# Performance work log

Hardware: AMD Instinct MI355X
Metric: run time of the kernel (lower is better)

Reference implementation:

```python
import jax, jax.numpy as jnp
import numpy as np

A, K, CIN, H, W = 8, 50, 64, 100, 352
C1, C2, C3, COUT = 128, 128, 256, 256


def setup_inputs() -> dict:
    key = jax.random.key(0)
    ks = jax.random.split(key, 16)

    def mkw(k, o, i, kh, kw):
        k1, k2 = jax.random.split(k)
        scale = (2.0 / (i * kh * kw)) ** 0.5 * 0.5  # damped He init to keep 8-layer relu stack stable
        return (jax.random.normal(k1, (o, i, kh, kw), jnp.float32) * scale,
                jax.random.normal(k2, (o,), jnp.float32) * 0.01)

    w1a, b1a = mkw(ks[0], C1, CIN, 3, 3)
    w1b, b1b = mkw(ks[1], C1, C1, 3, 3)
    w2a, b2a = mkw(ks[2], C2, C1, 3, 3)
    w2b, b2b = mkw(ks[3], C2, C2, 3, 3)
    w3a, b3a = mkw(ks[4], C3, C2, 3, 3)
    w3b, b3b = mkw(ks[5], C3, C3, 3, 3)
    wDa, bDa = mkw(ks[6], C3, C3, 3, 3)
    wDb, bDb = mkw(ks[7], COUT, C3, 1, 1)
    wF, bF = mkw(ks[8], COUT, COUT, 1, 1)

    feature = jax.random.normal(ks[9], (A, CIN, H, W), jnp.float32)

    # integer BEV boxes (left, right, up, down), right>left, down>up, vehicle-scale extents
    l = jax.random.randint(ks[10], (A, K), 0, W - 17)
    bw = jax.random.randint(ks[11], (A, K), 4, 17)
    u = jax.random.randint(ks[12], (A, K), 0, H - 17)
    bh = jax.random.randint(ks[13], (A, K), 4, 17)
    boxes = jnp.stack([l, l + bw, u, u + bh], axis=-1).astype(jnp.int32)  # [A,K,4]

    return dict(feature=feature, boxes=boxes,
                w1a=w1a, b1a=b1a, w1b=w1b, b1b=b1b,
                w2a=w2a, b2a=b2a, w2b=w2b, b2b=b2b,
                w3a=w3a, b3a=b3a, w3b=w3b, b3b=b3b,
                wDa=wDa, bDa=bDa, wDb=wDb, bDb=bDb,
                wF=wF, bF=bF)


def _conv(x, w, b, pad):
    y = jax.lax.conv_general_dilated(x, w, (1, 1), [(pad, pad), (pad, pad)],
                                     dimension_numbers=('NCHW', 'OIHW', 'NCHW'))
    return y + b[None, :, None, None]


def _superbox(feature, boxes, w1a, b1a, w1b, b1b, w2a, b2a, w2b, b2b,
              w3a, b3a, w3b, b3b, wDa, bDa, wDb, bDb, wF, bF):
    x = feature
    for (wi, bi) in ((w1a, b1a), (w1b, b1b), (w2a, b2a), (w2b, b2b),
                     (w3a, b3a), (w3b, b3b), (wDa, bDa)):
        x = jax.nn.relu(_conv(x, wi, bi, 1))
    x = jax.nn.relu(_conv(x, wDb, bDb, 0))        # [A,256,H,W] features_matching

    # get_box_feature: pool(relu(finalconv(crop))). finalconv is 1x1 (pointwise),
    # so this equals the box-mean of relu(finalconv(full map)) -> integral image.
    y = jax.nn.relu(_conv(x, wF, bF, 0))          # [A,256,H,W]
    S = jnp.pad(jnp.cumsum(jnp.cumsum(y, axis=2), axis=3),
                ((0, 0), (0, 0), (1, 0), (1, 0)))  # [A,256,H+1,W+1] integral image

    l, r, u, d = boxes[..., 0], boxes[..., 1], boxes[..., 2], boxes[..., 3]  # each [A,K]

    def agent_pool(Sa, la, ra, ua, da):
        # Sa: [C,H+1,W+1]; adjacent advanced indices -> [C,K]
        tot = Sa[:, da, ra] - Sa[:, ua, ra] - Sa[:, da, la] + Sa[:, ua, la]
        area = ((da - ua) * (ra - la)).astype(Sa.dtype)
        return (tot / area).T                     # [K,C]

    desc = jax.vmap(agent_pool)(S, l, r, u, d)    # [A,K,256]
    return desc


def reference(feature, boxes, w1a, b1a, w1b, b1b, w2a, b2a, w2b, b2b,
              w3a, b3a, w3b, b3b, wDa, bDa, wDb, bDb, wF, bF):
    return _superbox(feature, boxes, w1a, b1a, w1b, b1b, w2a, b2a, w2b, b2b,
                     w3a, b3a, w3b, b3b, wDa, bDa, wDb, bDb, wF, bF)
```

## Files before the change

kernel.cpp:

```cpp
#include <hip/hip_runtime.h>
#include <hip/hip_bf16.h>

typedef unsigned int u32;
typedef unsigned short u16;
typedef __attribute__((ext_vector_type(8))) short bf16x8;
typedef __attribute__((ext_vector_type(4))) float f32x4;

#define DEVI __device__ __forceinline__

constexpr int AG = 8, H = 100, W = 352, HP = 102, WP = 354;
constexpr int HWp = H * W;
constexpr int NB = 2 * WP + 2 * H;

DEVI u16 f2bf(float f) {
  __hip_bfloat16 h = __float2bfloat16(f);
  return *reinterpret_cast<u16*>(&h);
}
DEVI float bf2f(u16 v) { return __uint_as_float(((u32)v) << 16); }

DEVI int chperm(int j) { int v = j >> 3, r = j & 7; return (r < 4) ? 4 * v + r : 16 + 4 * v + (r - 4); }
DEVI int chlog(int c) { return (c & ~31) + chperm(c & 31); }

DEVI int xcd_lin(int orig, int nwg) {
  int q = nwg >> 3, r8 = nwg & 7;
  int xcd = orig & 7, pos = orig >> 3;
  return (xcd < r8 ? xcd * (q + 1) : r8 * (q + 1) + (xcd - r8) * q) + pos;
}

typedef __attribute__((address_space(1))) const u32 as1c_u32;
typedef __attribute__((address_space(3))) u32 as3_u32;
DEVI void gload16(const u16* g, u16* l) {
  __builtin_amdgcn_global_load_lds((as1c_u32*)(const void*)g, (as3_u32*)(void*)l, 16, 0, 0);
}

template <int N> DEVI void waitcnt_vm() {
  if constexpr (N == 0) asm volatile("s_waitcnt vmcnt(0)" ::: "memory");
  else if constexpr (N == 3) asm volatile("s_waitcnt vmcnt(3)" ::: "memory");
  else if constexpr (N == 4) asm volatile("s_waitcnt vmcnt(4)" ::: "memory");
  else asm volatile("s_waitcnt vmcnt(0)" ::: "memory");
}

__global__ void convert_feat(const float* __restrict__ f, u16* __restrict__ dst) {
  __shared__ float t32[64][33];
  int blk = blockIdx.x;
  int wseg = blk % 11;
  int rest = blk / 11;
  int h = rest % H;
  int a = rest / H;
  int t = threadIdx.x;
  int wbase = wseg * 32;
  {
    int w = t & 31;
    int c0 = (t >> 5) * 8;
#pragma unroll
    for (int i = 0; i < 8; ++i) {
      int lc = c0 + i;
      t32[lc][w] = f[((size_t)(a * 64 + lc) * H + h) * W + wbase + w];
    }
  }
  __syncthreads();
  int p = t >> 3;
  int cs = (t & 7) * 8;
  u16 tmp[8];
#pragma unroll
  for (int j = 0; j < 8; ++j) {
    int c = cs + j;
    int lc = (c & 32) + chperm(c & 31);
    tmp[j] = f2bf(t32[lc][p]);
  }
  size_t ob = ((size_t)(a * HP + h + 1) * WP + (wbase + p + 1)) * 64 + cs;
  *reinterpret_cast<uint4*>(dst + ob) = *reinterpret_cast<uint4*>(tmp);
}

template <int C>
__global__ void zero_border(u16* __restrict__ buf, int nA) {
  constexpr int CH = C / 8;
  int idx = blockIdx.x * 256 + threadIdx.x;
  int pix = idx / CH;
  int cc = (idx - pix * CH) * 8;
  if (pix >= nA * NB) return;
  int a = pix / NB;
  int b = pix - a * NB;
  int h, w;
  if (b < WP) { h = 0; w = b; }
  else if (b < 2 * WP) { h = HP - 1; w = b - WP; }
  else {
    int bb = b - 2 * WP;
    int bb2 = (bb < H) ? bb : bb - H;
    h = 1 + bb2;
    w = (bb < H) ? 0 : (WP - 1);
  }
  size_t off = ((size_t)(a * HP + h) * WP + w) * C + cc;
  *reinterpret_cast<uint4*>(buf + off) = make_uint4(0u, 0u, 0u, 0u);
}

__global__ void repack_w(const float* __restrict__ w, u16* __restrict__ rp,
                         int O, int I, int taps) {
  int idx = blockIdx.x * 256 + threadIdx.x;
  int total = O * I * taps;
  if (idx >= total) return;
  int jj = idx & 7;
  int u = (idx >> 3) & 7;
  int r = (idx >> 6) % O;
  int s = idx / (O * 64);
  int KB = I >> 6;
  int kb = s % KB;
  int t = s / KB;
  int lu = u ^ (r & 7);
  int g = lu & 3, j32 = lu >> 2;
  int cp = (jj < 4) ? 4 * g + jj : 16 + 4 * g + (jj - 4);
  int i = kb * 64 + j32 * 32 + cp;
  int o = (r & ~31) + chperm(r & 31);
  rp[idx] = f2bf(w[((size_t)o * I + i) * taps + t]);
}

__global__ void repack_plain(const float* __restrict__ w, u16* __restrict__ rp) {
  int idx = blockIdx.x * 256 + threadIdx.x;
  int jj = idx & 7;
  int g = (idx >> 3) & 3;
  int r = (idx >> 5) & 255;
  int kb = idx >> 13;
  int cp = (jj < 4) ? 4 * g + jj : 16 + 4 * g + (jj - 4);
  int i = kb * 32 + cp;
  int o = chlog(r);
  rp[idx] = f2bf(w[(size_t)o * 256 + i]);
}

template <int CIN, int COUT, int MAXCH, int HALO>
__global__ __launch_bounds__(256, 2) void conv_boxk(
    const u16* __restrict__ in, const u16* __restrict__ wrp,
    const float* __restrict__ bias, u16* __restrict__ out,
    const int* __restrict__ boxes) {
  constexpr int BM = 128, BN = 128, BK = 64, TAPS = 9;
  constexpr int KB = CIN / BK;
  constexpr int KS = TAPS * KB;
  constexpr int NT = 256;
  constexpr int NC = COUT / BN;
  constexpr int ACH = 4, AH = 2, BH = 2, HALF = 4;
  constexpr int ASZ = BM * BK;
  constexpr int BSZ = BN * BK;
  __shared__ u16 smem[2 * (ASZ + BSZ)];

  const int blk = xcd_lin(blockIdx.x, gridDim.x);
  const int cb = blk % NC;
  const int t1 = blk / NC;
  const int c0 = t1 % MAXCH;
  const int box = t1 / MAXCH;
  const int* bx = boxes + box * 4;
  const int a = box / 50;
  const int cl = max(bx[0] - HALO, 0);
  const int cr = min(bx[1] + HALO, W);
  const int r0 = max(bx[2] - HALO, 0);
  const int r1 = min(bx[3] + HALO, H);
  const int bw = cr - cl;
  const int npx = bw * (r1 - r0);
  if (c0 * 128 >= npx) return;

  const int tid = threadIdx.x;
  const int lane = tid & 63;
  const int wid = tid >> 6;
  const int wr = wid >> 1;
  const int wc = wid & 1;

  int aoff[ACH];
#pragma unroll
  for (int i = 0; i < ACH; ++i) {
    int c = tid + i * NT;
    int p = c >> 3, u = c & 7;
    int lu = u ^ (p & 7);
    int idx = c0 * 128 + p;
    if (idx >= npx) idx = npx - 1;
    int ph = r0 + idx / bw;
    int pw = cl + idx % bw;
    aoff[i] = ((a * HP + ph + 1) * WP + (pw + 1)) * CIN + lu * 8;
  }

  f32x4 acc[4][4];
#pragma unroll
  for (int m = 0; m < 4; ++m)
#pragma unroll
    for (int n = 0; n < 4; ++n) acc[m][n] = f32x4{0.f, 0.f, 0.f, 0.f};

  const int g = lane >> 4;
  const int arow = lane & 15;
  const int fk = arow & 7;

  auto stage = [&](int s, int h) {
    int par = s & 1;
    u16* Ad = smem + par * ASZ;
    u16* Bd = smem + 2 * ASZ + par * BSZ;
    int t = s / KB;
    int kb = s - t * KB;
    int doff = kb * BK + ((t / 3 - 1) * WP + (t % 3 - 1)) * CIN;
    const u16* wtile = wrp + (size_t)s * (COUT * BK) + cb * BSZ;
#pragma unroll
    for (int i = h * AH; i < h * AH + AH; ++i)
      gload16(in + aoff[i] + doff, Ad + (tid + i * NT) * 8);
#pragma unroll
    for (int i = h * BH; i < h * BH + BH; ++i)
      gload16(wtile + (tid + i * NT) * 8, Bd + (tid + i * NT) * 8);
  };

  stage(0, 0);
  stage(0, 1);

  for (int s = 0; s < KS; ++s) {
    int par = s & 1;
    const u16* Ab = smem + par * ASZ;
    const u16* Bb = smem + 2 * ASZ + par * BSZ;
    if (s + 1 < KS) {
      stage(s + 1, 0);
      waitcnt_vm<HALF>();
    } else {
      waitcnt_vm<0>();
    }
    __builtin_amdgcn_s_barrier();

#pragma unroll
    for (int j = 0; j < 2; ++j) {
      bf16x8 af[4], bfr[4];
#pragma unroll
      for (int m = 0; m < 4; ++m)
        af[m] = *reinterpret_cast<const bf16x8*>(
            Ab + (wr * 64 + m * 16 + arow) * 64 + (((j * 4 + g) ^ fk) << 3));
#pragma unroll
      for (int n = 0; n < 4; ++n)
        bfr[n] = *reinterpret_cast<const bf16x8*>(
            Bb + (wc * 64 + n * 16 + arow) * 64 + (((j * 4 + g) ^ fk) << 3));
      __builtin_amdgcn_s_setprio(1);
#pragma unroll
      for (int m = 0; m < 4; ++m)
#pragma unroll
        for (int n = 0; n < 4; ++n)
          acc[m][n] = __builtin_amdgcn_mfma_f32_16x16x32_bf16(af[m], bfr[n], acc[m][n], 0, 0, 0);
      __builtin_amdgcn_s_setprio(0);
      if (j == 0 && s + 1 < KS) stage(s + 1, 1);
    }
    __builtin_amdgcn_s_barrier();
  }

  __syncthreads();
  float bs[4];
#pragma unroll
  for (int n = 0; n < 4; ++n) bs[n] = bias[chlog(cb * BN + wc * 64 + n * 16 + arow)];
  u16* et = smem + wid * 2048;
#pragma unroll
  for (int pp = 0; pp < 2; ++pp) {
    if (pp) __syncthreads();
#pragma unroll
    for (int mm = 0; mm < 2; ++mm) {
      int m = pp * 2 + mm;
#pragma unroll
      for (int rg = 0; rg < 4; ++rg) {
        int row = mm * 16 + g * 4 + rg;
#pragma unroll
        for (int n = 0; n < 4; ++n) {
          int col = (n * 16 + arow) ^ (g << 4);
          et[row * 64 + col] = f2bf(fmaxf(acc[m][n][rg] + bs[n], 0.f));
        }
      }
    }
    __syncthreads();
#pragma unroll
    for (int jj = 0; jj < 4; ++jj) {
      int p = jj * 8 + (lane >> 3);
      int un = lane & 7;
      int su = un ^ (((p >> 2) & 3) << 1);
      uint4 qv = *reinterpret_cast<const uint4*>(et + p * 64 + su * 8);
      int idx = c0 * 128 + wr * 64 + pp * 32 + p;
      if (idx >= npx) idx = npx - 1;
      int ph = r0 + idx / bw;
      int pw = cl + idx % bw;
      size_t ob = ((size_t)(a * HP + ph + 1) * WP + (pw + 1)) * COUT +
                  cb * BN + wc * 64 + un * 8;
      *reinterpret_cast<uint4*>(out + ob) = qv;
    }
  }
}

template <int CIN, int EOUT, int MAXCH, int MODE>
__global__ __launch_bounds__(256, 2) void conv_tl(
    const u16* __restrict__ in, const u16* __restrict__ wrp,
    const float* __restrict__ bias, u16* __restrict__ out,
    const int* __restrict__ boxes) {
  constexpr int BM = 128, BN = 128, BK = 64, TAPS = 9;
  constexpr int KB = CIN / BK;
  constexpr int KS = TAPS * KB;
  constexpr int NT = 256;
  constexpr int NC = 2;
  constexpr int COUT = 256;
  constexpr int ACH = 4, AH = 2, BH = 2, HALF = 4;
  constexpr int ASZ = BM * BK;
  constexpr int BSZ = BN * BK;
  constexpr int TSLOT = (MODE == 0) ? 400 : (MODE == 1) ? 324 : 256;
  constexpr int TIN_SLOT = (MODE == 1) ? 400 : (MODE == 2) ? 324 : 0;
  __shared__ u16 smem[2 * (ASZ + BSZ)];

  const int blk = xcd_lin(blockIdx.x, gridDim.x);
  const int cb = blk % NC;
  const int t1 = blk / NC;
  const int c0 = t1 % MAXCH;
  const int box = t1 / MAXCH;
  const int* bx = boxes + box * 4;
  const int a = box / 50;
  const int bw = bx[1] - bx[0], bh = bx[3] - bx[2];
  const int bwO = bw + 2 * EOUT, bhO = bh + 2 * EOUT;
  const int NPX = bwO * bhO;
  if (c0 * 128 >= NPX) return;
  const int org_r = bx[2] - EOUT, org_c = bx[0] - EOUT;
  const int bwIn = bw + 2 * (EOUT + 1);

  const int tid = threadIdx.x;
  const int lane = tid & 63;
  const int wid = tid >> 6;
  const int wr = wid >> 1;
  const int wc = wid & 1;

  const u16* src = (MODE == 0) ? in : in + (size_t)box * TIN_SLOT * CIN;

  int aoff[ACH];
#pragma unroll
  for (int i = 0; i < ACH; ++i) {
    int c = tid + i * NT;
    int p = c >> 3, u = c & 7;
    int lu = u ^ (p & 7);
    int idx = c0 * 128 + p;
    if (idx >= NPX) idx = NPX - 1;
    int r = idx / bwO, cc = idx - r * bwO;
    if (MODE == 0) {
      int mr = org_r + r, mc = org_c + cc;
      mr = min(max(mr, 0), H - 1);
      mc = min(max(mc, 0), W - 1);
      aoff[i] = ((a * HP + mr + 1) * WP + (mc + 1)) * CIN + lu * 8;
    } else {
      aoff[i] = ((r + 1) * bwIn + (cc + 1)) * CIN + lu * 8;
    }
  }

  f32x4 acc[4][4];
#pragma unroll
  for (int m = 0; m < 4; ++m)
#pragma unroll
    for (int n = 0; n < 4; ++n) acc[m][n] = f32x4{0.f, 0.f, 0.f, 0.f};

  const int g = lane >> 4;
  const int arow = lane & 15;
  const int fk = arow & 7;
  const int stride = (MODE == 0) ? WP : bwIn;

  auto stage = [&](int s, int h) {
    int par = s & 1;
    u16* Ad = smem + par * ASZ;
    u16* Bd = smem + 2 * ASZ + par * BSZ;
    int t = s / KB;
    int kb = s - t * KB;
    int doff = kb * BK + ((t / 3 - 1) * stride + (t % 3 - 1)) * CIN;
    const u16* wtile = wrp + (size_t)s * (COUT * BK) + cb * BSZ;
#pragma unroll
    for (int i = h * AH; i < h * AH + AH; ++i)
      gload16(src + aoff[i] + doff, Ad + (tid + i * NT) * 8);
#pragma unroll
    for (int i = h * BH; i < h * BH + BH; ++i)
      gload16(wtile + (tid + i * NT) * 8, Bd + (tid + i * NT) * 8);
  };

  stage(0, 0);
  stage(0, 1);

  for (int s = 0; s < KS; ++s) {
    int par = s & 1;
    const u16* Ab = smem + par * ASZ;
    const u16* Bb = smem + 2 * ASZ + par * BSZ;
    if (s + 1 < KS) {
      stage(s + 1, 0);
      waitcnt_vm<HALF>();
    } else {
      waitcnt_vm<0>();
    }
    __builtin_amdgcn_s_barrier();

#pragma unroll
    for (int j = 0; j < 2; ++j) {
      bf16x8 af[4], bfr[4];
#pragma unroll
      for (int m = 0; m < 4; ++m)
        af[m] = *reinterpret_cast<const bf16x8*>(
            Ab + (wr * 64 + m * 16 + arow) * 64 + (((j * 4 + g) ^ fk) << 3));
#pragma unroll
      for (int n = 0; n < 4; ++n)
        bfr[n] = *reinterpret_cast<const bf16x8*>(
            Bb + (wc * 64 + n * 16 + arow) * 64 + (((j * 4 + g) ^ fk) << 3));
      __builtin_amdgcn_s_setprio(1);
#pragma unroll
      for (int m = 0; m < 4; ++m)
#pragma unroll
        for (int n = 0; n < 4; ++n)
          acc[m][n] = __builtin_amdgcn_mfma_f32_16x16x32_bf16(af[m], bfr[n], acc[m][n], 0, 0, 0);
      __builtin_amdgcn_s_setprio(0);
      if (j == 0 && s + 1 < KS) stage(s + 1, 1);
    }
    __builtin_amdgcn_s_barrier();
  }

  __syncthreads();
  float bs[4];
#pragma unroll
  for (int n = 0; n < 4; ++n) bs[n] = bias[chlog(cb * BN + wc * 64 + n * 16 + arow)];
  u16* et = smem + wid * 2048;
#pragma unroll
  for (int pp = 0; pp < 2; ++pp) {
    if (pp) __syncthreads();
#pragma unroll
    for (int mm = 0; mm < 2; ++mm) {
      int m = pp * 2 + mm;
#pragma unroll
      for (int rg = 0; rg < 4; ++rg) {
        int row = mm * 16 + g * 4 + rg;
#pragma unroll
        for (int n = 0; n < 4; ++n) {
          int col = (n * 16 + arow) ^ (g << 4);
          et[row * 64 + col] = f2bf(fmaxf(acc[m][n][rg] + bs[n], 0.f));
        }
      }
    }
    __syncthreads();
#pragma unroll
    for (int jj = 0; jj < 4; ++jj) {
      int p = jj * 8 + (lane >> 3);
      int un = lane & 7;
      int su = un ^ (((p >> 2) & 3) << 1);
      uint4 qv = *reinterpret_cast<const uint4*>(et + p * 64 + su * 8);
      int idx = c0 * 128 + wr * 64 + pp * 32 + p;
      if (idx >= NPX) idx = NPX - 1;
      if (MODE != 2) {
        int r2 = idx / bwO, c2 = idx - (idx / bwO) * bwO;
        int mr = org_r + r2, mc = org_c + c2;
        if (mr < 0 || mr >= H || mc < 0 || mc >= W)
          qv = make_uint4(0u, 0u, 0u, 0u);
      }
      size_t ob = ((size_t)box * TSLOT + idx) * COUT + cb * BN + wc * 64 + un * 8;
      *reinterpret_cast<uint4*>(out + ob) = qv;
    }
  }
}

__global__ __launch_bounds__(256) void fuse_box(
    const u16* __restrict__ x, const u16* __restrict__ wDbp,
    const float* __restrict__ bDb, const u16* __restrict__ wFp,
    const float* __restrict__ bF, const int* __restrict__ boxes,
    float* __restrict__ desc) {
  __shared__ u16 xT[16 * 256];
  const int blk = blockIdx.x;
  const int* bx = boxes + blk * 4;
  const int bw = bx[1] - bx[0];
  const int npx = bw * (bx[3] - bx[2]);
  const int nch = (npx + 15) >> 4;
  const int tid = threadIdx.x;
  const int lane = tid & 63;
  const int wc = tid >> 6;
  const int g = lane >> 4;
  const int arow = lane & 15;

  float b1[4], b2[4];
#pragma unroll
  for (int nf = 0; nf < 4; ++nf) {
    int ch = wc * 64 + nf * 16 + arow;
    b1[nf] = bDb[chlog(ch)];
    b2[nf] = bF[chlog(ch)];
  }
  float sums[4] = {0.f, 0.f, 0.f, 0.f};

  for (int ci = 0; ci < nch; ++ci) {
    int idx = ci * 16 + arow;
    if (idx >= npx) idx = npx - 1;
    const u16* ap = x + ((size_t)blk * 256 + idx) * 256;
    f32x4 a1[4];
#pragma unroll
    for (int nf = 0; nf < 4; ++nf) a1[nf] = f32x4{0.f, 0.f, 0.f, 0.f};
#pragma unroll
    for (int kb = 0; kb < 8; ++kb) {
      bf16x8 af = *reinterpret_cast<const bf16x8*>(ap + kb * 32 + g * 8);
#pragma unroll
      for (int nf = 0; nf < 4; ++nf) {
        bf16x8 bf_ = *reinterpret_cast<const bf16x8*>(
            wDbp + (((size_t)kb * 256 + wc * 64 + nf * 16 + arow) * 4 + g) * 8);
        a1[nf] = __builtin_amdgcn_mfma_f32_16x16x32_bf16(af, bf_, a1[nf], 0, 0, 0);
      }
    }
    if (ci) __syncthreads();
#pragma unroll
    for (int nf = 0; nf < 4; ++nf)
#pragma unroll
      for (int rg = 0; rg < 4; ++rg) {
        int px = g * 4 + rg;
        int ch = wc * 64 + nf * 16 + arow;
        int siu = (ch >> 3) ^ (px & 7);
        xT[px * 256 + siu * 8 + (ch & 7)] = f2bf(fmaxf(a1[nf][rg] + b1[nf], 0.f));
      }
    __syncthreads();
    f32x4 a2[4];
#pragma unroll
    for (int nf = 0; nf < 4; ++nf) a2[nf] = f32x4{0.f, 0.f, 0.f, 0.f};
#pragma unroll
    for (int kb = 0; kb < 8; ++kb) {
      int iu = kb * 4 + g;
      bf16x8 af2 = *reinterpret_cast<const bf16x8*>(
          xT + arow * 256 + (iu ^ (arow & 7)) * 8);
#pragma unroll
      for (int nf = 0; nf < 4; ++nf) {
        bf16x8 bf_ = *reinterpret_cast<const bf16x8*>(
            wFp + (((size_t)kb * 256 + wc * 64 + nf * 16 + arow) * 4 + g) * 8);
        a2[nf] = __builtin_amdgcn_mfma_f32_16x16x32_bf16(af2, bf_, a2[nf], 0, 0, 0);
      }
    }
#pragma unroll
    for (int nf = 0; nf < 4; ++nf)
#pragma unroll
      for (int rg = 0; rg < 4; ++rg) {
        int pidx = ci * 16 + g * 4 + rg;
        if (pidx < npx) sums[nf] += fmaxf(a2[nf][rg] + b2[nf], 0.f);
      }
  }
#pragma unroll
  for (int nf = 0; nf < 4; ++nf) {
    sums[nf] += __shfl_xor(sums[nf], 16, 64);
    sums[nf] += __shfl_xor(sums[nf], 32, 64);
  }
  if (g == 0) {
    float inv = 1.f / (float)npx;
#pragma unroll
    for (int nf = 0; nf < 4; ++nf) {
      int ch = wc * 64 + nf * 16 + arow;
      desc[(size_t)blk * 256 + chlog(ch)] = sums[nf] * inv;
    }
  }
}

extern "C" void kernel_launch(void* const* d_in, const int* in_sizes, int n_in,
                              void* d_out, int out_size, void* d_ws, size_t ws_size,
                              hipStream_t stream) {
  const float* feature = (const float*)d_in[0];
  const int* boxes = (const int*)d_in[1];
  const float* w1a = (const float*)d_in[2];
  const float* b1a = (const float*)d_in[3];
  const float* w1b = (const float*)d_in[4];
  const float* b1b = (const float*)d_in[5];
  const float* w2a = (const float*)d_in[6];
  const float* b2a = (const float*)d_in[7];
  const float* w2b = (const float*)d_in[8];
  const float* b2b = (const float*)d_in[9];
  const float* w3a = (const float*)d_in[10];
  const float* b3a = (const float*)d_in[11];
  const float* w3b = (const float*)d_in[12];
  const float* b3b = (const float*)d_in[13];
  const float* wDa = (const float*)d_in[14];
  const float* bDa = (const float*)d_in[15];
  const float* wDb = (const float*)d_in[16];
  const float* bDb = (const float*)d_in[17];
  const float* wF = (const float*)d_in[18];
  const float* bF = (const float*)d_in[19];

  const size_t e1a = (size_t)9 * 64 * 128;
  const size_t e128 = (size_t)9 * 128 * 128;
  const size_t e3a = (size_t)9 * 128 * 256;
  const size_t e256 = (size_t)9 * 256 * 256;
  const size_t ePl = (size_t)256 * 256;
  const size_t WELEMS = e1a + 3 * e128 + e3a + 2 * e256 + 2 * ePl;
  const size_t WB = WELEMS * 2;
  const size_t PER_A = (size_t)320 * HP * WP * 2;
  int aloc = (ws_size >= 8 * PER_A + WB) ? 8 : (ws_size >= 4 * PER_A + WB) ? 4 : 2;

  char* ws = (char*)d_ws;
  const size_t SZ64  = (size_t)aloc * HP * WP * 64 * 2;
  const size_t SZ128 = (size_t)aloc * HP * WP * 128 * 2;
  const size_t SZ192 = SZ64 + SZ128;
  u16* in64 = (u16*)(ws);
  u16* X    = (u16*)(ws + SZ64);
  u16* T0   = (u16*)(ws);
  u16* T2   = (u16*)(ws);
  u16* Y    = (u16*)(ws + SZ192);
  u16* T1   = (u16*)(ws + SZ192);
  u16* rp   = (u16*)(ws + SZ192 + SZ128);

  const size_t o1a = 0;
  const size_t o1b = o1a + e1a;
  const size_t o2a = o1b + e128;
  const size_t o2b = o2a + e128;
  const size_t o3a = o2b + e128;
  const size_t o3b = o3a + e3a;
  const size_t oDa = o3b + e256;
  const size_t oDbP = oDa + e256;
  const size_t oFP = oDbP + ePl;

  auto rpk = [&](const float* wsrc, size_t off, int O, int I, int taps) {
    int total = O * I * taps;
    repack_w<<<(total + 255) / 256, 256, 0, stream>>>(wsrc, rp + off, O, I, taps);
  };
  rpk(w1a, o1a, 128, 64, 9);
  rpk(w1b, o1b, 128, 128, 9);
  rpk(w2a, o2a, 128, 128, 9);
  rpk(w2b, o2b, 128, 128, 9);
  rpk(w3a, o3a, 256, 128, 9);
  rpk(w3b, o3b, 256, 256, 9);
  rpk(wDa, oDa, 256, 256, 9);
  repack_plain<<<256, 256, 0, stream>>>(wDb, rp + oDbP);
  repack_plain<<<256, 256, 0, stream>>>(wF, rp + oFP);

  const int nbox = aloc * 50;
  for (int a0 = 0; a0 < AG; a0 += aloc) {
    const int* bxs = boxes + (size_t)a0 * 50 * 4;
    zero_border<64><<<(aloc * NB * 8 + 255) / 256, 256, 0, stream>>>(in64, aloc);
    zero_border<128><<<(aloc * NB * 16 + 255) / 256, 256, 0, stream>>>(X, aloc);
    zero_border<128><<<(aloc * NB * 16 + 255) / 256, 256, 0, stream>>>(Y, aloc);

    convert_feat<<<aloc * H * 11, 256, 0, stream>>>(
        feature + (size_t)a0 * 64 * H * W, in64);

    conv_boxk<64, 128, 7, 6><<<nbox * 7, 256, 0, stream>>>(in64, rp + o1a, b1a, X, bxs);
    conv_boxk<128, 128, 6, 5><<<nbox * 6, 256, 0, stream>>>(X, rp + o1b, b1b, Y, bxs);
    conv_boxk<128, 128, 5, 4><<<nbox * 5, 256, 0, stream>>>(Y, rp + o2a, b2a, X, bxs);
    conv_boxk<128, 128, 4, 3><<<nbox * 4, 256, 0, stream>>>(X, rp + o2b, b2b, Y, bxs);
    conv_tl<128, 2, 4, 0><<<nbox * 4 * 2, 256, 0, stream>>>(Y, rp + o3a, b3a, T0, bxs);
    conv_tl<256, 1, 3, 1><<<nbox * 3 * 2, 256, 0, stream>>>(T0, rp + o3b, b3b, T1, bxs);
    conv_tl<256, 0, 2, 2><<<nbox * 2 * 2, 256, 0, stream>>>(T1, rp + oDa, bDa, T2, bxs);
    fuse_box<<<nbox, 256, 0, stream>>>(
        T2, rp + oDbP, bDb, rp + oFP, bF, bxs,
        ((float*)d_out) + (size_t)a0 * 50 * 256);
  }
}
```

Before: 628.9 us.

## Triple-buffer activation tiles and prefetch two stages ahead in conv kernels

Splits the tile loader into separate activation and weight stages. The activation (gathered, latency-heavy) tile now gets a three-slot LDS ring and is prefetched two k-steps ahead, while weights stay double-buffered one step ahead. The vmcnt waits are adjusted to the deeper queue. This is meant to hide global gather latency better, at the cost of more LDS per block (about 80KB), which may limit the two-blocks-per-CU occupancy.

```diff
diff --git a/kernel.cpp b/kernel.cpp
--- a/kernel.cpp
+++ b/kernel.cpp
@@ -35,8 +35,9 @@
 
 template <int N> DEVI void waitcnt_vm() {
   if constexpr (N == 0) asm volatile("s_waitcnt vmcnt(0)" ::: "memory");
-  else if constexpr (N == 3) asm volatile("s_waitcnt vmcnt(3)" ::: "memory");
   else if constexpr (N == 4) asm volatile("s_waitcnt vmcnt(4)" ::: "memory");
+  else if constexpr (N == 8) asm volatile("s_waitcnt vmcnt(8)" ::: "memory");
+  else if constexpr (N == 12) asm volatile("s_waitcnt vmcnt(12)" ::: "memory");
   else asm volatile("s_waitcnt vmcnt(0)" ::: "memory");
 }
 
@@ -136,10 +137,10 @@
   constexpr int KS = TAPS * KB;
   constexpr int NT = 256;
   constexpr int NC = COUT / BN;
-  constexpr int ACH = 4, AH = 2, BH = 2, HALF = 4;
+  constexpr int ACH = 4;
   constexpr int ASZ = BM * BK;
   constexpr int BSZ = BN * BK;
-  __shared__ u16 smem[2 * (ASZ + BSZ)];
+  __shared__ u16 smem[3 * ASZ + 2 * BSZ];
 
   const int blk = xcd_lin(blockIdx.x, gridDim.x);
   const int cb = blk % NC;
@@ -185,35 +186,35 @@
   const int arow = lane & 15;
   const int fk = arow & 7;
 
-  auto stage = [&](int s, int h) {
-    int par = s & 1;
-    u16* Ad = smem + par * ASZ;
-    u16* Bd = smem + 2 * ASZ + par * BSZ;
+  auto stageA = [&](int s) {
+    u16* Ad = smem + (s % 3) * ASZ;
     int t = s / KB;
     int kb = s - t * KB;
     int doff = kb * BK + ((t / 3 - 1) * WP + (t % 3 - 1)) * CIN;
+#pragma unroll
+    for (int i = 0; i < ACH; ++i)
+      gload16(in + aoff[i] + doff, Ad + (tid + i * NT) * 8);
+  };
+  auto stageB = [&](int s) {
+    u16* Bd = smem + 3 * ASZ + (s & 1) * BSZ;
     const u16* wtile = wrp + (size_t)s * (COUT * BK) + cb * BSZ;
 #pragma unroll
-    for (int i = h * AH; i < h * AH + AH; ++i)
-      gload16(in + aoff[i] + doff, Ad + (tid + i * NT) * 8);
-#pragma unroll
-    for (int i = h * BH; i < h * BH + BH; ++i)
+    for (int i = 0; i < 4; ++i)
       gload16(wtile + (tid + i * NT) * 8, Bd + (tid + i * NT) * 8);
   };
 
-  stage(0, 0);
-  stage(0, 1);
+  stageB(0);
+  stageA(0);
+  if (KS > 1) stageA(1);
 
   for (int s = 0; s < KS; ++s) {
-    int par = s & 1;
-    const u16* Ab = smem + par * ASZ;
-    const u16* Bb = smem + 2 * ASZ + par * BSZ;
-    if (s + 1 < KS) {
-      stage(s + 1, 0);
-      waitcnt_vm<HALF>();
-    } else {
-      waitcnt_vm<0>();
-    }
+    const u16* Ab = smem + (s % 3) * ASZ;
+    const u16* Bb = smem + 3 * ASZ + (s & 1) * BSZ;
+    if (s + 1 < KS) stageB(s + 1);
+    if (s + 2 < KS) stageA(s + 2);
+    if (s + 2 < KS) waitcnt_vm<12>();
+    else if (s + 1 < KS) waitcnt_vm<8>();
+    else waitcnt_vm<0>();
     __builtin_amdgcn_s_barrier();
 
 #pragma unroll
@@ -234,7 +235,6 @@
         for (int n = 0; n < 4; ++n)
           acc[m][n] = __builtin_amdgcn_mfma_f32_16x16x32_bf16(af[m], bfr[n], acc[m][n], 0, 0, 0);
       __builtin_amdgcn_s_setprio(0);
-      if (j == 0 && s + 1 < KS) stage(s + 1, 1);
     }
     __builtin_amdgcn_s_barrier();
   }
@@ -289,12 +289,12 @@
   constexpr int NT = 256;
   constexpr int NC = 2;
   constexpr int COUT = 256;
-  constexpr int ACH = 4, AH = 2, BH = 2, HALF = 4;
+  constexpr int ACH = 4;
   constexpr int ASZ = BM * BK;
   constexpr int BSZ = BN * BK;
   constexpr int TSLOT = (MODE == 0) ? 400 : (MODE == 1) ? 324 : 256;
   constexpr int TIN_SLOT = (MODE == 1) ? 400 : (MODE == 2) ? 324 : 0;
-  __shared__ u16 smem[2 * (ASZ + BSZ)];
+  __shared__ u16 smem[3 * ASZ + 2 * BSZ];
 
   const int blk = xcd_lin(blockIdx.x, gridDim.x);
   const int cb = blk % NC;
@@ -348,35 +348,35 @@
   const int fk = arow & 7;
   const int stride = (MODE == 0) ? WP : bwIn;
 
-  auto stage = [&](int s, int h) {
-    int par = s & 1;
-    u16* Ad = smem + par * ASZ;
-    u16* Bd = smem + 2 * ASZ + par * BSZ;
+  auto stageA = [&](int s) {
+    u16* Ad = smem + (s % 3) * ASZ;
     int t = s / KB;
     int kb = s - t * KB;
     int doff = kb * BK + ((t / 3 - 1) * stride + (t % 3 - 1)) * CIN;
+#pragma unroll
+    for (int i = 0; i < ACH; ++i)
+      gload16(src + aoff[i] + doff, Ad + (tid + i * NT) * 8);
+  };
+  auto stageB = [&](int s) {
+    u16* Bd = smem + 3 * ASZ + (s & 1) * BSZ;
     const u16* wtile = wrp + (size_t)s * (COUT * BK) + cb * BSZ;
 #pragma unroll
-    for (int i = h * AH; i < h * AH + AH; ++i)
-      gload16(src + aoff[i] + doff, Ad + (tid + i * NT) * 8);
-#pragma unroll
-    for (int i = h * BH; i < h * BH + BH; ++i)
+    for (int i = 0; i < 4; ++i)
       gload16(wtile + (tid + i * NT) * 8, Bd + (tid + i * NT) * 8);
   };
 
-  stage(0, 0);
-  stage(0, 1);
+  stageB(0);
+  stageA(0);
+  if (KS > 1) stageA(1);
 
   for (int s = 0; s < KS; ++s) {
-    int par = s & 1;
-    const u16* Ab = smem + par * ASZ;
-    const u16* Bb = smem + 2 * ASZ + par * BSZ;
-    if (s + 1 < KS) {
-      stage(s + 1, 0);
-      waitcnt_vm<HALF>();
-    } else {
-      waitcnt_vm<0>();
-    }
+    const u16* Ab = smem + (s % 3) * ASZ;
+    const u16* Bb = smem + 3 * ASZ + (s & 1) * BSZ;
+    if (s + 1 < KS) stageB(s + 1);
+    if (s + 2 < KS) stageA(s + 2);
+    if (s + 2 < KS) waitcnt_vm<12>();
+    else if (s + 1 < KS) waitcnt_vm<8>();
+    else waitcnt_vm<0>();
     __builtin_amdgcn_s_barrier();
 
 #pragma unroll
@@ -397,7 +397,6 @@
         for (int n = 0; n < 4; ++n)
           acc[m][n] = __builtin_amdgcn_mfma_f32_16x16x32_bf16(af[m], bfr[n], acc[m][n], 0, 0, 0);
       __builtin_amdgcn_s_setprio(0);
-      if (j == 0 && s + 1 < KS) stage(s + 1, 1);
     }
     __builtin_amdgcn_s_barrier();
   }
```

Measured after the change: 628.9 us. No clear change (+0.0%).
